# Optimization experiments

Hardware: AMD Instinct MI355X
Metric: run time of the kernel (lower is better)

Reference implementation:

```python
import jax, jax.numpy as jnp
import numpy as np

B, T, H = 1024, 1024, 64


def _lstm_cell(x, h, c, w_ih, w_hh, b_ih, b_hh):
    # gates: [B, 4H] in PyTorch order i, f, g, o
    g = x @ w_ih.T + h @ w_hh.T + b_ih + b_hh
    i, f, gg, o = jnp.split(g, 4, axis=-1)
    i = jax.nn.sigmoid(i)
    f = jax.nn.sigmoid(f)
    gg = jnp.tanh(gg)
    o = jax.nn.sigmoid(o)
    c_new = f * c + i * gg
    h_new = o * jnp.tanh(c_new)
    return h_new, c_new


def setup_inputs() -> dict:
    key = jax.random.key(0)
    ks = jax.random.split(key, 12)
    s = 1.0 / np.sqrt(H)  # torch default init scale
    r = lambda k, shape: jax.random.normal(k, shape, dtype=jnp.float32) * s
    return {
        "x": jax.random.normal(ks[0], (B, T), dtype=jnp.float32),
        "w_ih1": r(ks[1], (4 * H, 1)),
        "w_hh1": r(ks[2], (4 * H, H)),
        "b_ih1": r(ks[3], (4 * H,)),
        "b_hh1": r(ks[4], (4 * H,)),
        "w_ih2": r(ks[5], (4 * H, H)),
        "w_hh2": r(ks[6], (4 * H, H)),
        "b_ih2": r(ks[7], (4 * H,)),
        "b_hh2": r(ks[8], (4 * H,)),
        "w_lin": r(ks[9], (1, H)),
        "b_lin": r(ks[10], (1,)),
        "future_preds": 0,
    }


def reference(x, w_ih1, w_hh1, b_ih1, b_hh1, w_ih2, w_hh2, b_ih2, b_hh2,
              w_lin, b_lin, future_preds):
    bsz = x.shape[0]
    h1 = jnp.zeros((bsz, H), x.dtype)
    c1 = jnp.zeros((bsz, H), x.dtype)
    h2 = jnp.zeros((bsz, H), x.dtype)
    c2 = jnp.zeros((bsz, H), x.dtype)

    def step(carry, x_t):
        h1, c1, h2, c2 = carry
        h1, c1 = _lstm_cell(x_t, h1, c1, w_ih1, w_hh1, b_ih1, b_hh1)
        h2, c2 = _lstm_cell(h1, h2, c2, w_ih2, w_hh2, b_ih2, b_hh2)
        out = h2 @ w_lin.T + b_lin  # [B, 1]
        return (h1, c1, h2, c2), out

    xs = x.T[:, :, None]  # [T, B, 1]
    carry, outs = jax.lax.scan(step, (h1, c1, h2, c2), xs)
    outputs = outs[:, :, 0].T  # [B, T]

    if future_preds > 0:
        last = outs[-1]  # [B, 1]

        def fstep(carry, _):
            h1, c1, h2, c2, prev = carry
            h1, c1 = _lstm_cell(prev, h1, c1, w_ih1, w_hh1, b_ih1, b_hh1)
            h2, c2 = _lstm_cell(h1, h2, c2, w_ih2, w_hh2, b_ih2, b_hh2)
            out = h2 @ w_lin.T + b_lin
            return (h1, c1, h2, c2, out), out

        _, fouts = jax.lax.scan(fstep, (*carry, last), None, length=future_preds)
        outputs = jnp.concatenate([outputs, fouts[:, :, 0].T], axis=1)

    return outputs
```

## Files before the change

### kernel.cpp

```cpp
#include <hip/hip_runtime.h>
#include <hip/hip_bf16.h>


typedef _Float16 f16x8 __attribute__((ext_vector_type(8)));
typedef float    f32x4 __attribute__((ext_vector_type(4)));

namespace {
constexpr int Bb = 1024;
constexpr int Tt = 1024;
constexpr int NBat = 4;
constexpr int HSTR = 72;
constexpr int XSTR = 1025;

__device__ __forceinline__ int srow(int row) {
    return row ^ ((row >> 3) & 7);
}
__device__ __forceinline__ float sigm(float x) {
    float e = __builtin_amdgcn_exp2f(-1.4426950408889634f * x);
    return __builtin_amdgcn_rcpf(1.0f + e);
}
__device__ __forceinline__ float tanh_f(float x) {
    float e = __builtin_amdgcn_exp2f(-2.8853900817779268f * x);
    return __builtin_amdgcn_rcpf(1.0f + e) * 2.0f - 1.0f;
}
__device__ __forceinline__ bool detect_f32(const void* w) {
    const unsigned short* p = (const unsigned short*)w;
    int sane = 0;
    for (int i = 0; i < 64; ++i) {
        int e = (p[2 * i] >> 7) & 0xFF;
        if (e >= 107 && e <= 129) ++sane;
    }
    return sane < 32;
}
__device__ __forceinline__ float ld(const void* p, int i, bool f32) {
    return f32 ? ((const float*)p)[i]
               : __bfloat162float(((const __hip_bfloat16*)p)[i]);
}
__device__ __forceinline__ void st(void* p, int i, float v, bool f32) {
    if (f32) ((float*)p)[i] = v;
    else     ((__hip_bfloat16*)p)[i] = __float2bfloat16(v);
}
}

__global__ __launch_bounds__(512, 1) void lstm2_kernel(
    const void* __restrict__ x,
    const void* __restrict__ w_ih1,
    const void* __restrict__ w_hh1,
    const void* __restrict__ b_ih1,
    const void* __restrict__ b_hh1,
    const void* __restrict__ w_ih2,
    const void* __restrict__ w_hh2,
    const void* __restrict__ b_ih2,
    const void* __restrict__ b_hh2,
    const void* __restrict__ w_lin,
    const void* __restrict__ b_lin,
    void* __restrict__ out)
{
    const int tid  = threadIdx.x;
    const int lane = tid & 63;
    const int w    = tid >> 6;
    const int gw   = w & 3;
    const bool isP = w < 4;
    const int m    = lane & 15;
    const int quad = lane >> 4;
    const int bb   = blockIdx.x * NBat;

    const bool f32 = detect_f32(w_hh1);

    __shared__ float                  xs[NBat * XSTR];
    __shared__ __align__(16) _Float16 h1buf[2][16 * HSTR];
    __shared__ __align__(16) _Float16 h2buf[2][16 * HSTR];
    __shared__ __align__(16) float    scr1[4][64 * 4];
    __shared__ __align__(16) float    scr2[4][64 * 4];
    __shared__ float                  headl[2][16];

    for (int i = tid; i < NBat * 1024; i += 512)
        xs[(i >> 10) * XSTR + (i & 1023)] = ld(x, (bb + (i >> 10)) * Tt + (i & 1023), f32);
    for (int i = tid; i < 16 * HSTR; i += 512) {
        h1buf[0][i] = (_Float16)0; h1buf[1][i] = (_Float16)0;
        h2buf[0][i] = (_Float16)0; h2buf[1][i] = (_Float16)0;
    }

    const int arow = lane & 15;
    const int g_ld = arow & 3;
    const int u_ld = arow >> 2;
    f16x8 wfA[4][2], wfB[4][2];
    {
        const void* MA = isP ? w_hh1 : w_ih2;
#pragma unroll
        for (int q = 0; q < 4; ++q) {
            const int row = 64 * g_ld + 16 * gw + 4 * q + u_ld;
#pragma unroll
            for (int s = 0; s < 2; ++s) {
                const int base = row * 64 + 32 * s + quad * 8;
                if (f32) {
                    const float* A = (const float*)MA;
                    const float* B = (const float*)w_hh2;
#pragma unroll
                    for (int j = 0; j < 8; ++j) {
                        wfA[q][s][j] = (_Float16)A[base + j];
                        wfB[q][s][j] = isP ? (_Float16)0.0f : (_Float16)B[base + j];
                    }
                } else {
                    const __hip_bfloat16* A = (const __hip_bfloat16*)MA;
                    const __hip_bfloat16* B = (const __hip_bfloat16*)w_hh2;
#pragma unroll
                    for (int j = 0; j < 8; ++j) {
                        wfA[q][s][j] = (_Float16)__bfloat162float(A[base + j]);
                        wfB[q][s][j] = isP ? (_Float16)0.0f
                                           : (_Float16)__bfloat162float(B[base + j]);
                    }
                }
            }
        }
    }
    f32x4 bv[4], wxv[4];
#pragma unroll
    for (int q = 0; q < 4; ++q)
#pragma unroll
        for (int r = 0; r < 4; ++r) {
            const int row = 64 * r + 16 * gw + 4 * q + quad;
            bv[q][r] = isP ? (ld(b_ih1, row, f32) + ld(b_hh1, row, f32))
                           : (ld(b_ih2, row, f32) + ld(b_hh2, row, f32));
            wxv[q][r] = isP ? ld(w_ih1, row, f32) : 0.0f;
        }
    const int cb = lane >> 4;
    const int uo = lane & 15;
    const int cidx = srow(lane) * 4;
    const float wl_u = ld(w_lin, 16 * gw + uo, f32);
    const float blin = ld(b_lin, 0, f32);
    float cst = 0.0f;
    __syncthreads();

    for (int t = 0; t <= Tt; ++t) {
        if (isP) {
            if (t < Tt) {
                f32x4 acc[4];
                const float xt = xs[(m & (NBat - 1)) * XSTR + t];
#pragma unroll
                for (int q = 0; q < 4; ++q)
#pragma unroll
                    for (int r = 0; r < 4; ++r)
                        acc[q][r] = fmaf(xt, wxv[q][r], bv[q][r]);
                if (t > 0) {
                    const _Float16* hp = h1buf[(t - 1) & 1] + m * HSTR;
                    const f16x8 ba = *(const f16x8*)(hp + quad * 8);
                    const f16x8 bb2 = *(const f16x8*)(hp + 32 + quad * 8);
#pragma unroll
                    for (int q = 0; q < 4; ++q) {
                        acc[q] = __builtin_amdgcn_mfma_f32_16x16x32_f16(wfA[q][0], ba, acc[q], 0, 0, 0);
                        acc[q] = __builtin_amdgcn_mfma_f32_16x16x32_f16(wfA[q][1], bb2, acc[q], 0, 0, 0);
                    }
                }
                if (m < NBat)
#pragma unroll
                    for (int q = 0; q < 4; ++q)
                        *(f32x4*)&scr1[gw][srow(m * 16 + q * 4 + quad) * 4] = acc[q];
                const f32x4 g = *(const f32x4*)&scr1[gw][cidx];
                float ig = sigm(g[0]), fg = sigm(g[1]);
                float gg = tanh_f(g[2]), og = sigm(g[3]);
                cst = fmaf(fg, cst, ig * gg);
                h1buf[t & 1][cb * HSTR + 16 * gw + uo] = (_Float16)(og * tanh_f(cst));
            }
        } else {
            if (t > 0) {
                if (t > 1 && w == 4 && lane < NBat) {
                    float s = blin;
#pragma unroll
                    for (int k = 0; k < 4; ++k) s += headl[t & 1][k * 4 + lane];
                    st(out, (bb + lane) * Tt + (t - 2), s, f32);
                }
                const _Float16* h1p = h1buf[(t - 1) & 1] + m * HSTR;
                const _Float16* h2p = h2buf[t & 1] + m * HSTR;
                const f16x8 b1a = *(const f16x8*)(h1p + quad * 8);
                const f16x8 b1b = *(const f16x8*)(h1p + 32 + quad * 8);
                const f16x8 b2a = *(const f16x8*)(h2p + quad * 8);
                const f16x8 b2b = *(const f16x8*)(h2p + 32 + quad * 8);
                f32x4 acc[4];
#pragma unroll
                for (int q = 0; q < 4; ++q) {
                    f32x4 p = __builtin_amdgcn_mfma_f32_16x16x32_f16(wfA[q][0], b1a, bv[q], 0, 0, 0);
                    p = __builtin_amdgcn_mfma_f32_16x16x32_f16(wfA[q][1], b1b, p, 0, 0, 0);
                    p = __builtin_amdgcn_mfma_f32_16x16x32_f16(wfB[q][0], b2a, p, 0, 0, 0);
                    acc[q] = __builtin_amdgcn_mfma_f32_16x16x32_f16(wfB[q][1], b2b, p, 0, 0, 0);
                }
                if (m < NBat)
#pragma unroll
                    for (int q = 0; q < 4; ++q)
                        *(f32x4*)&scr2[gw][srow(m * 16 + q * 4 + quad) * 4] = acc[q];
                const f32x4 g = *(const f32x4*)&scr2[gw][cidx];
                float ig = sigm(g[0]), fg = sigm(g[1]);
                float gg = tanh_f(g[2]), og = sigm(g[3]);
                cst = fmaf(fg, cst, ig * gg);
                float h = og * tanh_f(cst);
                h2buf[(t - 1) & 1][cb * HSTR + 16 * gw + uo] = (_Float16)h;
                float p = h * wl_u;
                p += __shfl_xor(p, 1); p += __shfl_xor(p, 2);
                p += __shfl_xor(p, 4); p += __shfl_xor(p, 8);
                if (uo == 0) headl[(t - 1) & 1][gw * 4 + cb] = p;
            }
        }
        __syncthreads();
    }

    if (w == 4 && lane < NBat) {
        float s = blin;
#pragma unroll
        for (int k = 0; k < 4; ++k) s += headl[(Tt - 1) & 1][k * 4 + lane];
        st(out, (bb + lane) * Tt + (Tt - 1), s, f32);
    }
}

extern "C" void kernel_launch(void* const* d_in, const int* in_sizes, int n_in,
                              void* d_out, int out_size, void* d_ws, size_t ws_size,
                              hipStream_t stream)
{
    (void)in_sizes; (void)n_in; (void)out_size; (void)d_ws; (void)ws_size;
    lstm2_kernel<<<dim3(Bb / NBat), dim3(512), 0, stream>>>(
        d_in[0], d_in[1], d_in[2], d_in[3], d_in[4], d_in[5],
        d_in[6], d_in[7], d_in[8], d_in[9], d_in[10], d_out);
}
```

Measured before the change: 826.2 us.

## Replace per-step block barrier with LDS flag counters between layer wave groups

Replaces the per-timestep __syncthreads with workgroup-scope atomic counters in shared memory. Layer-1 waves bump pdone and layer-2 waves bump qdone, and each group spin-waits (with s_sleep) only on the step counts it depends on. The h1 buffer grows to four slots so layer 1 can run up to three steps ahead of layer 2, decoupling the two recurrences. The trade is spin-polling latency and more subtle memory-ordering requirements in exchange for removing the lockstep barrier.

Result: slower. 938.4 us (+13.6%).

```diff
diff --git a/kernel.cpp b/kernel.cpp
--- a/kernel.cpp
+++ b/kernel.cpp
@@ -39,6 +39,15 @@
 __device__ __forceinline__ void st(void* p, int i, float v, bool f32) {
     if (f32) ((float*)p)[i] = v;
     else     ((__hip_bfloat16*)p)[i] = __float2bfloat16(v);
+}
+__device__ __forceinline__ void spin_ge(unsigned* f, unsigned need) {
+    while (__hip_atomic_load(f, __ATOMIC_ACQUIRE,
+                             __HIP_MEMORY_SCOPE_WORKGROUP) < need)
+        __builtin_amdgcn_s_sleep(1);
+}
+__device__ __forceinline__ void bump(unsigned* f) {
+    __hip_atomic_fetch_add(f, 1u, __ATOMIC_RELEASE,
+                           __HIP_MEMORY_SCOPE_WORKGROUP);
 }
 }
 
@@ -68,18 +77,21 @@
     const bool f32 = detect_f32(w_hh1);
 
     __shared__ float                  xs[NBat * XSTR];
-    __shared__ __align__(16) _Float16 h1buf[2][16 * HSTR];
+    __shared__ __align__(16) _Float16 h1buf[4][16 * HSTR];
     __shared__ __align__(16) _Float16 h2buf[2][16 * HSTR];
     __shared__ __align__(16) float    scr1[4][64 * 4];
     __shared__ __align__(16) float    scr2[4][64 * 4];
     __shared__ float                  headl[2][16];
+    __shared__ unsigned               pdone, qdone;
 
     for (int i = tid; i < NBat * 1024; i += 512)
         xs[(i >> 10) * XSTR + (i & 1023)] = ld(x, (bb + (i >> 10)) * Tt + (i & 1023), f32);
     for (int i = tid; i < 16 * HSTR; i += 512) {
         h1buf[0][i] = (_Float16)0; h1buf[1][i] = (_Float16)0;
+        h1buf[2][i] = (_Float16)0; h1buf[3][i] = (_Float16)0;
         h2buf[0][i] = (_Float16)0; h2buf[1][i] = (_Float16)0;
     }
+    if (tid == 0) { pdone = 0u; qdone = 0u; }
 
     const int arow = lane & 15;
     const int g_ld = arow & 3;
@@ -132,82 +144,87 @@
     float cst = 0.0f;
     __syncthreads();
 
-    for (int t = 0; t <= Tt; ++t) {
-        if (isP) {
-            if (t < Tt) {
-                f32x4 acc[4];
-                const float xt = xs[(m & (NBat - 1)) * XSTR + t];
+    if (isP) {
+        for (int t = 0; t < Tt; ++t) {
+            if (t >= 1) spin_ge(&pdone, 4u * t);
+            if (t >= 4) spin_ge(&qdone, 4u * (t - 3));
+            f32x4 acc[4];
+            const float xt = xs[(m & (NBat - 1)) * XSTR + t];
+#pragma unroll
+            for (int q = 0; q < 4; ++q)
+#pragma unroll
+                for (int r = 0; r < 4; ++r)
+                    acc[q][r] = fmaf(xt, wxv[q][r], bv[q][r]);
+            if (t > 0) {
+                const _Float16* hp = h1buf[(t - 1) & 3] + m * HSTR;
+                const f16x8 ba = *(const f16x8*)(hp + quad * 8);
+                const f16x8 bb2 = *(const f16x8*)(hp + 32 + quad * 8);
+#pragma unroll
+                for (int q = 0; q < 4; ++q) {
+                    acc[q] = __builtin_amdgcn_mfma_f32_16x16x32_f16(wfA[q][0], ba, acc[q], 0, 0, 0);
+                    acc[q] = __builtin_amdgcn_mfma_f32_16x16x32_f16(wfA[q][1], bb2, acc[q], 0, 0, 0);
+                }
+            }
+            if (m < NBat)
 #pragma unroll
                 for (int q = 0; q < 4; ++q)
-#pragma unroll
-                    for (int r = 0; r < 4; ++r)
-                        acc[q][r] = fmaf(xt, wxv[q][r], bv[q][r]);
-                if (t > 0) {
-                    const _Float16* hp = h1buf[(t - 1) & 1] + m * HSTR;
-                    const f16x8 ba = *(const f16x8*)(hp + quad * 8);
-                    const f16x8 bb2 = *(const f16x8*)(hp + 32 + quad * 8);
-#pragma unroll
-                    for (int q = 0; q < 4; ++q) {
-                        acc[q] = __builtin_amdgcn_mfma_f32_16x16x32_f16(wfA[q][0], ba, acc[q], 0, 0, 0);
-                        acc[q] = __builtin_amdgcn_mfma_f32_16x16x32_f16(wfA[q][1], bb2, acc[q], 0, 0, 0);
-                    }
-                }
-                if (m < NBat)
-#pragma unroll
-                    for (int q = 0; q < 4; ++q)
-                        *(f32x4*)&scr1[gw][srow(m * 16 + q * 4 + quad) * 4] = acc[q];
-                const f32x4 g = *(const f32x4*)&scr1[gw][cidx];
-                float ig = sigm(g[0]), fg = sigm(g[1]);
-                float gg = tanh_f(g[2]), og = sigm(g[3]);
-                cst = fmaf(fg, cst, ig * gg);
-                h1buf[t & 1][cb * HSTR + 16 * gw + uo] = (_Float16)(og * tanh_f(cst));
-            }
-        } else {
-            if (t > 0) {
-                if (t > 1 && w == 4 && lane < NBat) {
-                    float s = blin;
-#pragma unroll
-                    for (int k = 0; k < 4; ++k) s += headl[t & 1][k * 4 + lane];
-                    st(out, (bb + lane) * Tt + (t - 2), s, f32);
-                }
-                const _Float16* h1p = h1buf[(t - 1) & 1] + m * HSTR;
-                const _Float16* h2p = h2buf[t & 1] + m * HSTR;
-                const f16x8 b1a = *(const f16x8*)(h1p + quad * 8);
-                const f16x8 b1b = *(const f16x8*)(h1p + 32 + quad * 8);
-                const f16x8 b2a = *(const f16x8*)(h2p + quad * 8);
-                const f16x8 b2b = *(const f16x8*)(h2p + 32 + quad * 8);
-                f32x4 acc[4];
-#pragma unroll
-                for (int q = 0; q < 4; ++q) {
-                    f32x4 p = __builtin_amdgcn_mfma_f32_16x16x32_f16(wfA[q][0], b1a, bv[q], 0, 0, 0);
-                    p = __builtin_amdgcn_mfma_f32_16x16x32_f16(wfA[q][1], b1b, p, 0, 0, 0);
-                    p = __builtin_amdgcn_mfma_f32_16x16x32_f16(wfB[q][0], b2a, p, 0, 0, 0);
-                    acc[q] = __builtin_amdgcn_mfma_f32_16x16x32_f16(wfB[q][1], b2b, p, 0, 0, 0);
-                }
-                if (m < NBat)
-#pragma unroll
-                    for (int q = 0; q < 4; ++q)
-                        *(f32x4*)&scr2[gw][srow(m * 16 + q * 4 + quad) * 4] = acc[q];
-                const f32x4 g = *(const f32x4*)&scr2[gw][cidx];
-                float ig = sigm(g[0]), fg = sigm(g[1]);
-                float gg = tanh_f(g[2]), og = sigm(g[3]);
-                cst = fmaf(fg, cst, ig * gg);
-                float h = og * tanh_f(cst);
-                h2buf[(t - 1) & 1][cb * HSTR + 16 * gw + uo] = (_Float16)h;
-                float p = h * wl_u;
-                p += __shfl_xor(p, 1); p += __shfl_xor(p, 2);
-                p += __shfl_xor(p, 4); p += __shfl_xor(p, 8);
-                if (uo == 0) headl[(t - 1) & 1][gw * 4 + cb] = p;
-            }
-        }
-        __syncthreads();
-    }
-
-    if (w == 4 && lane < NBat) {
-        float s = blin;
-#pragma unroll
-        for (int k = 0; k < 4; ++k) s += headl[(Tt - 1) & 1][k * 4 + lane];
-        st(out, (bb + lane) * Tt + (Tt - 1), s, f32);
+                    *(f32x4*)&scr1[gw][srow(m * 16 + q * 4 + quad) * 4] = acc[q];
+            const f32x4 g = *(const f32x4*)&scr1[gw][cidx];
+            float ig = sigm(g[0]), fg = sigm(g[1]);
+            float gg = tanh_f(g[2]), og = sigm(g[3]);
+            cst = fmaf(fg, cst, ig * gg);
+            h1buf[t & 3][cb * HSTR + 16 * gw + uo] = (_Float16)(og * tanh_f(cst));
+            if (lane == 0) bump(&pdone);
+        }
+    } else {
+        for (int s = 0; s < Tt; ++s) {
+            spin_ge(&pdone, 4u * (s + 1));
+            if (s >= 1) spin_ge(&qdone, 4u * s);
+            if (s >= 1 && w == 4 && lane < NBat) {
+                float sum = blin;
+#pragma unroll
+                for (int k = 0; k < 4; ++k) sum += headl[(s - 1) & 1][k * 4 + lane];
+                st(out, (bb + lane) * Tt + (s - 1), sum, f32);
+            }
+            const _Float16* h1p = h1buf[s & 3] + m * HSTR;
+            const _Float16* h2p = h2buf[(s - 1) & 1] + m * HSTR;
+            const f16x8 b1a = *(const f16x8*)(h1p + quad * 8);
+            const f16x8 b1b = *(const f16x8*)(h1p + 32 + quad * 8);
+            const f16x8 b2a = *(const f16x8*)(h2p + quad * 8);
+            const f16x8 b2b = *(const f16x8*)(h2p + 32 + quad * 8);
+            f32x4 acc[4];
+#pragma unroll
+            for (int q = 0; q < 4; ++q) {
+                f32x4 p = __builtin_amdgcn_mfma_f32_16x16x32_f16(wfA[q][0], b1a, bv[q], 0, 0, 0);
+                p = __builtin_amdgcn_mfma_f32_16x16x32_f16(wfA[q][1], b1b, p, 0, 0, 0);
+                p = __builtin_amdgcn_mfma_f32_16x16x32_f16(wfB[q][0], b2a, p, 0, 0, 0);
+                acc[q] = __builtin_amdgcn_mfma_f32_16x16x32_f16(wfB[q][1], b2b, p, 0, 0, 0);
+            }
+            if (m < NBat)
+#pragma unroll
+                for (int q = 0; q < 4; ++q)
+                    *(f32x4*)&scr2[gw][srow(m * 16 + q * 4 + quad) * 4] = acc[q];
+            const f32x4 g = *(const f32x4*)&scr2[gw][cidx];
+            float ig = sigm(g[0]), fg = sigm(g[1]);
+            float gg = tanh_f(g[2]), og = sigm(g[3]);
+            cst = fmaf(fg, cst, ig * gg);
+            float h = og * tanh_f(cst);
+            h2buf[s & 1][cb * HSTR + 16 * gw + uo] = (_Float16)h;
+            float p = h * wl_u;
+            p += __shfl_xor(p, 1); p += __shfl_xor(p, 2);
+            p += __shfl_xor(p, 4); p += __shfl_xor(p, 8);
+            if (uo == 0) headl[s & 1][gw * 4 + cb] = p;
+            if (lane == 0) bump(&qdone);
+        }
+        if (w == 4) {
+            spin_ge(&qdone, 4u * Tt);
+            if (lane < NBat) {
+                float sum = blin;
+#pragma unroll
+                for (int k = 0; k < 4; ++k) sum += headl[(Tt - 1) & 1][k * 4 + lane];
+                st(out, (bb + lane) * Tt + (Tt - 1), sum, f32);
+            }
+        }
     }
 }
 
```
